# Kernel optimization log

Hardware: AMD Instinct MI355X
Metric: run time of the kernel (lower is better)

The kernel has to match this reference:

```python
import jax, jax.numpy as jnp
import numpy as np

N = 50000          # nodes
E = 1250000        # edges (no self loops in raw data)
H = 2              # heads
C = 32             # out channels per head
DIN = 64           # dim_node
ED = 16            # edge_dim
G = 16             # graphs in batch
NC = 5             # num classes
SLOPE = 0.2        # GATConv leaky_relu negative_slope


def _glorot(key, shape):
    fan = shape[0] if len(shape) == 2 else shape[-1]
    return jax.random.normal(key, shape, jnp.float32) * (1.0 / np.sqrt(fan))


def setup_inputs() -> dict:
    key = jax.random.key(0)
    ks = jax.random.split(key, 24)
    x = jax.random.normal(ks[0], (N, DIN), jnp.float32)
    dst = jax.random.randint(ks[1], (E,), 0, N)
    off = jax.random.randint(ks[2], (E,), 1, N)
    src = (dst + off) % N  # guarantees src != dst (PyG removes self loops before re-adding)
    edge_index = jnp.stack([src, dst]).astype(jnp.int32)
    edge_attr = jax.random.normal(ks[3], (E, ED), jnp.float32)
    batch = jnp.sort(jax.random.randint(ks[4], (N,), 0, G)).astype(jnp.int32)
    inp = dict(x=x, edge_index=edge_index, edge_attr=edge_attr, batch=batch)
    # layer 1: in=DIN, heads=H, out=C, concat -> H*C
    inp["W1"] = _glorot(ks[5], (DIN, H * C)); inp["asrc1"] = _glorot(ks[6], (H, C))
    inp["adst1"] = _glorot(ks[7], (H, C)); inp["We1"] = _glorot(ks[8], (ED, H * C))
    inp["ae1"] = _glorot(ks[9], (H, C)); inp["b1"] = jnp.zeros((H * C,), jnp.float32)
    # layer 2: in=H*C, heads=H, out=C, concat
    inp["W2"] = _glorot(ks[10], (H * C, H * C)); inp["asrc2"] = _glorot(ks[11], (H, C))
    inp["adst2"] = _glorot(ks[12], (H, C)); inp["We2"] = _glorot(ks[13], (ED, H * C))
    inp["ae2"] = _glorot(ks[14], (H, C)); inp["b2"] = jnp.zeros((H * C,), jnp.float32)
    # layer 3: in=H*C, heads=1, out=C, concat=False
    inp["W3"] = _glorot(ks[15], (H * C, C)); inp["asrc3"] = _glorot(ks[16], (1, C))
    inp["adst3"] = _glorot(ks[17], (1, C)); inp["We3"] = _glorot(ks[18], (ED, C))
    inp["ae3"] = _glorot(ks[19], (1, C)); inp["b3"] = jnp.zeros((C,), jnp.float32)
    # ffn: Linear(C, NC) + softmax (dropout is identity in eval)
    inp["Wf"] = _glorot(ks[20], (C, NC)); inp["bf"] = jnp.zeros((NC,), jnp.float32)
    return inp


def _gat_layer(h_in, src, dst, eattr, W, asrc, adst, We, ae, b, heads, out, concat):
    n = h_in.shape[0]
    h = (h_in @ W).reshape(n, heads, out)                      # [N,H,C]
    s_src = jnp.einsum('nhc,hc->nh', h, asrc)                  # per-node src scores
    s_dst = jnp.einsum('nhc,hc->nh', h, adst)
    he = (eattr @ We).reshape(-1, heads, out)                  # [E,H,C]
    s_e = jnp.einsum('ehc,hc->eh', he, ae)
    logit = jax.nn.leaky_relu(s_src[src] + s_dst[dst] + s_e, SLOPE)  # [E,H]
    m = jax.ops.segment_max(logit, dst, num_segments=n)
    ex = jnp.exp(logit - m[dst])
    den = jax.ops.segment_sum(ex, dst, num_segments=n)
    alpha = ex / (den[dst] + 1e-16)                            # segment softmax per dst node
    agg = jax.ops.segment_sum(h[src] * alpha[..., None], dst, num_segments=n)  # [N,H,C]
    out_x = agg.reshape(n, heads * out) if concat else agg.mean(axis=1)
    return out_x + b


def _gat_forward(x, edge_index, edge_attr, batch,
                 W1, asrc1, adst1, We1, ae1, b1,
                 W2, asrc2, adst2, We2, ae2, b2,
                 W3, asrc3, adst3, We3, ae3, b3,
                 Wf, bf):
    src, dst = edge_index[0], edge_index[1]
    n = x.shape[0]
    # add_self_loops with fill_value='mean': self-loop edge_attr = mean of incoming edge_attr
    deg = jax.ops.segment_sum(jnp.ones((src.shape[0],), x.dtype), dst, num_segments=n)
    self_attr = jax.ops.segment_sum(edge_attr, dst, num_segments=n) / jnp.maximum(deg, 1.0)[:, None]
    loop = jnp.arange(n, dtype=src.dtype)
    src_a = jnp.concatenate([src, loop])
    dst_a = jnp.concatenate([dst, loop])
    eattr_a = jnp.concatenate([edge_attr, self_attr], axis=0)

    h = jax.nn.relu(_gat_layer(x, src_a, dst_a, eattr_a, W1, asrc1, adst1, We1, ae1, b1, H, C, True))
    h = jax.nn.relu(_gat_layer(h, src_a, dst_a, eattr_a, W2, asrc2, adst2, We2, ae2, b2, H, C, True))
    h = jax.nn.relu(_gat_layer(h, src_a, dst_a, eattr_a, W3, asrc3, adst3, We3, ae3, b3, 1, C, False))

    # global mean pool per graph
    cnt = jax.ops.segment_sum(jnp.ones((n,), h.dtype), batch, num_segments=G)
    pooled = jax.ops.segment_sum(h, batch, num_segments=G) / jnp.maximum(cnt, 1.0)[:, None]
    # ffn: Dropout (identity at eval) -> Linear -> Softmax(dim=1)
    return jax.nn.softmax(pooled @ Wf + bf, axis=1)


def reference(x, edge_index, edge_attr, batch,
              W1, asrc1, adst1, We1, ae1, b1,
              W2, asrc2, adst2, We2, ae2, b2,
              W3, asrc3, adst3, We3, ae3, b3,
              Wf, bf):
    return _gat_forward(x, edge_index, edge_attr, batch,
                        W1, asrc1, adst1, We1, ae1, b1,
                        W2, asrc2, adst2, We2, ae2, b2,
                        W3, asrc3, adst3, We3, ae3, b3,
                        Wf, bf)
```

## Files before the change

### kernel.cpp

```cpp
#include <hip/hip_runtime.h>
#include <math.h>

#define NN 50000
#define EE 1250000
#define GG 16
#define NCLS 5
#define NBIN 391
#define BINSHIFT 7
#define CAPB 3900

constexpr size_t AL(size_t x){ return (x + 255) & ~size_t(255); }
constexpr size_t OFF_ROWPTR = 0;
constexpr size_t OFF_SRCS   = OFF_ROWPTR + AL((size_t)(NN+1)*4);
constexpr size_t OFF_SE12   = OFF_SRCS + AL((size_t)EE*2);
constexpr size_t OFF_SE34   = OFF_SE12 + AL((size_t)EE*4);
constexpr size_t OFF_SE5    = OFF_SE34 + AL((size_t)EE*4);
constexpr size_t OFF_SSRC   = OFF_SE5 + AL((size_t)EE*2);
constexpr size_t OFF_SDST   = OFF_SSRC + AL((size_t)NN*2*4);
constexpr size_t OFF_STAG   = OFF_SDST + AL((size_t)NN*2*4);
constexpr size_t OFF_BUFH   = OFF_STAG + AL((size_t)NBIN*CAPB*16);
constexpr size_t OFF_BUFO   = OFF_BUFH + AL((size_t)NN*32*4);
constexpr size_t OFF_POOL   = OFF_BUFO + AL((size_t)NN*64*4);

__device__ __forceinline__ float leaky(float x){ return x > 0.f ? x : 0.2f*x; }
__device__ __forceinline__ unsigned rne_bf16(float x){
    unsigned u = __float_as_uint(x);
    return (u + 0x7FFFu + ((u >> 16) & 1u)) >> 16;
}
__device__ __forceinline__ float bf16lo(unsigned p){ return __uint_as_float(p << 16); }
__device__ __forceinline__ float bf16hi(unsigned p){ return __uint_as_float(p & 0xFFFF0000u); }

__global__ void binA_kernel(const int* __restrict__ src, const int* __restrict__ dst,
                            const float* __restrict__ eattr,
                            const float* __restrict__ We1, const float* __restrict__ ae1,
                            const float* __restrict__ We2, const float* __restrict__ ae2,
                            const float* __restrict__ We3, const float* __restrict__ ae3,
                            int* __restrict__ bincursor, int4* __restrict__ staging, int nE){
    __shared__ int lcount[NBIN];
    __shared__ int lbase[NBIN];
    __shared__ float w[80];
    int tid = threadIdx.x;
    if (tid < 80){
        int j = tid >> 4, d = tid & 15;
        const float* We; const float* ae; int hc, h;
        if (j == 0){ We = We1; ae = ae1; hc = 64; h = 0; }
        else if (j == 1){ We = We1; ae = ae1; hc = 64; h = 1; }
        else if (j == 2){ We = We2; ae = ae2; hc = 64; h = 0; }
        else if (j == 3){ We = We2; ae = ae2; hc = 64; h = 1; }
        else { We = We3; ae = ae3; hc = 32; h = 0; }
        float s = 0.f;
        for (int c = 0; c < 32; ++c) s += We[d*hc + h*32 + c] * ae[h*32 + c];
        w[tid] = s;
    }
    for (int i = tid; i < NBIN; i += 1024) lcount[i] = 0;
    __syncthreads();
    int base = blockIdx.x * 2048;
    int w0[2], bn[2], idx[2]; unsigned p01[2], p23[2], p4[2];
    #pragma unroll
    for (int k = 0; k < 2; ++k){
        int i = base + k*1024 + tid;
        if (i < nE){
            int d = dst[i];
            int s = src[i];
            bn[k]  = d >> BINSHIFT;
            w0[k]  = s | ((d & 127) << 16);
            const float4* row = (const float4*)(eattr + (size_t)i*16);
            float4 a0 = row[0], a1 = row[1], a2 = row[2], a3 = row[3];
            float a[16] = {a0.x,a0.y,a0.z,a0.w, a1.x,a1.y,a1.z,a1.w,
                           a2.x,a2.y,a2.z,a2.w, a3.x,a3.y,a3.z,a3.w};
            float sj[5];
            #pragma unroll
            for (int j = 0; j < 5; ++j){
                float s2 = 0.f;
                #pragma unroll
                for (int d2 = 0; d2 < 16; ++d2) s2 += a[d2]*w[j*16+d2];
                sj[j] = s2;
            }
            p01[k] = rne_bf16(sj[0]) | (rne_bf16(sj[1]) << 16);
            p23[k] = rne_bf16(sj[2]) | (rne_bf16(sj[3]) << 16);
            p4[k]  = rne_bf16(sj[4]);
            idx[k] = atomicAdd(&lcount[bn[k]], 1);
        } else bn[k] = -1;
    }
    __syncthreads();
    for (int i = tid; i < NBIN; i += 1024){
        int c = lcount[i];
        lbase[i] = c ? (i*CAPB + atomicAdd(&bincursor[i], c)) : 0;
    }
    __syncthreads();
    #pragma unroll
    for (int k = 0; k < 2; ++k)
        if (bn[k] >= 0)
            staging[lbase[bn[k]] + idx[k]] = make_int4(w0[k], (int)p01[k], (int)p23[k], (int)p4[k]);
}

__global__ void binB_kernel(const int* __restrict__ bincursor, const int4* __restrict__ staging,
                            unsigned short* __restrict__ srcs, unsigned* __restrict__ se12,
                            unsigned* __restrict__ se34, unsigned short* __restrict__ se5,
                            int* __restrict__ rowptr, int nN){
    __shared__ int4 lout[CAPB];
    __shared__ int lcnt[128];
    __shared__ int lpre[128];
    __shared__ int sbb;
    int b = blockIdx.x;
    int sbase = b*CAPB;
    int cnt = bincursor[b];
    int tid = threadIdx.x;
    if (tid < 128) lcnt[tid] = 0;
    if (tid < 64){
        int sum = 0;
        for (int i = tid; i < b; i += 64) sum += bincursor[i];
        #pragma unroll
        for (int m = 1; m < 64; m <<= 1) sum += __shfl_xor(sum, m);
        if (tid == 0) sbb = sum;
    }
    __syncthreads();
    for (int k = tid; k < cnt; k += 1024)
        atomicAdd(&lcnt[staging[sbase + k].x >> 16], 1);
    __syncthreads();
    if (tid < 64){
        int a0 = lcnt[2*tid], a1 = lcnt[2*tid+1];
        int pair = a0 + a1, incl = pair;
        #pragma unroll
        for (int off = 1; off < 64; off <<= 1){
            int t = __shfl_up(incl, off);
            if (tid >= off) incl += t;
        }
        int base0 = incl - pair;
        lpre[2*tid] = base0;
        lpre[2*tid+1] = base0 + a0;
    }
    __syncthreads();
    int r0 = sbb;
    int lo = b << BINSHIFT;
    if (tid < 128 && lo + tid < nN) rowptr[lo + tid] = r0 + lpre[tid];
    if (b == 0 && tid == 0) rowptr[nN] = EE;
    if (tid < 128) lcnt[tid] = 0;
    __syncthreads();
    for (int k = tid; k < cnt; k += 1024){
        int4 v = staging[sbase + k];
        int dl = v.x >> 16;
        int rank = atomicAdd(&lcnt[dl], 1);
        v.x &= 0xFFFF;
        lout[lpre[dl] + rank] = v;
    }
    __syncthreads();
    for (int k = tid; k < cnt; k += 1024){
        int4 v = lout[k];
        srcs[r0 + k] = (unsigned short)v.x;
        se12[r0 + k] = (unsigned)v.y;
        se34[r0 + k] = (unsigned)v.z;
        se5[r0 + k]  = (unsigned short)v.w;
    }
}

template<int OUTC>
__global__ void transform_kernel(const float* __restrict__ in, const float* __restrict__ W,
                                 const float* __restrict__ asrc, const float* __restrict__ adst,
                                 unsigned* __restrict__ hout2, float* __restrict__ ssrc,
                                 float* __restrict__ sdst, int nN){
    constexpr int R = 256/OUTC;
    __shared__ float Ws[64*OUTC];
    __shared__ float ins[R*64];
    int tid = threadIdx.x;
    for (int i = tid; i < 64*OUTC; i += 256) Ws[i] = W[i];
    int base = blockIdx.x * R;
    for (int i = tid; i < R*64; i += 256){
        int n = base + i/64;
        ins[i] = (n < nN) ? in[(size_t)n*64 + (i & 63)] : 0.f;
    }
    __syncthreads();
    int r = tid / OUTC, c = tid % OUTC;
    int n = base + r;
    float acc = 0.f;
    #pragma unroll
    for (int d = 0; d < 64; ++d) acc += ins[r*64 + d] * Ws[d*OUTC + c];
    float ps = acc * asrc[c];
    float pd = acc * adst[c];
    #pragma unroll
    for (int m = 1; m <= 16; m <<= 1){ ps += __shfl_xor(ps, m); pd += __shfl_xor(pd, m); }
    float accN = __shfl_xor(acc, 1);
    if (n < nN){
        if ((c & 1) == 0){
            unsigned pk = rne_bf16(acc) | (rne_bf16(accN) << 16);
            hout2[(size_t)n*(OUTC/2) + (c >> 1)] = pk;
        }
        constexpr int HEADS = OUTC/32;
        if ((c & 31) == 0){
            int h = c >> 5;
            ssrc[n*HEADS + h] = ps;
            sdst[n*HEADS + h] = pd;
        }
    }
}

template<int OUTC>
__global__ void agg_kernel(const int* __restrict__ rowptr, const unsigned short* __restrict__ srcs,
                           const unsigned* __restrict__ sePa, const unsigned short* __restrict__ sePb,
                           const float* __restrict__ ssrc, const float* __restrict__ sdst,
                           const unsigned* __restrict__ hbuf2, const float* __restrict__ bias,
                           float* __restrict__ outbuf, int nN){
    constexpr int HEADS = OUTC/32;
    constexpr int HALF  = OUTC/4;
    constexpr int EPI   = 64/HALF;
    int wid = threadIdx.x >> 6;
    int lane = threadIdx.x & 63;
    int n = blockIdx.x*4 + wid;
    if (n >= nN) return;
    int row_start = rowptr[n], row_end = rowptr[n+1];
    int degn = row_end - row_start;
    float sd0 = sdst[n*HEADS + 0];
    float sd1 = (HEADS == 2) ? sdst[n*HEADS + 1] : 0.f;

    int sub = lane / HALF;
    int lc  = lane & (HALF - 1);
    int h   = (HEADS == 2) ? ((4*lc) >> 5) : 0;

    float acc0=0.f, acc1=0.f, acc2=0.f, acc3=0.f, den=0.f;
    float ssp0=0.f, ssp1=0.f;
    const uint2* hb2 = (const uint2*)hbuf2;

    for (int p0 = row_start; p0 < row_end; p0 += 64){
        int myp = p0 + lane;
        int srcreg = 0; unsigned wpk = 0; float w0s = 0.f;
        if (myp < row_end){
            srcreg = srcs[myp];
            if (HEADS == 2){
                unsigned pk = sePa[myp];
                float e0 = bf16lo(pk);
                float e1 = bf16hi(pk);
                ssp0 += e0; ssp1 += e1;
                float2 sv = ((const float2*)ssrc)[srcreg];
                float w0 = __expf(leaky(sv.x + sd0 + e0));
                float w1 = __expf(leaky(sv.y + sd1 + e1));
                wpk = rne_bf16(w0) | (rne_bf16(w1) << 16);
            } else {
                float e0 = __uint_as_float(((unsigned)sePb[myp]) << 16);
                ssp0 += e0;
                w0s = __expf(leaky(ssrc[srcreg] + sd0 + e0));
            }
        }
        int cnt = min(64, row_end - p0);
        #pragma unroll 2
        for (int q = sub; q < cnt; q += EPI){
            int sj = __shfl(srcreg, q);
            float wj;
            if (HEADS == 2){
                unsigned wq = __shfl(wpk, q);
                wj = h ? bf16hi(wq) : bf16lo(wq);
            } else {
                wj = __shfl(w0s, q);
            }
            den += wj;
            uint2 hv = hb2[(size_t)sj*(OUTC/4) + lc];
            acc0 += wj * bf16lo(hv.x);
            acc1 += wj * bf16hi(hv.x);
            acc2 += wj * bf16lo(hv.y);
            acc3 += wj * bf16hi(hv.y);
        }
    }

    #pragma unroll
    for (int m = HALF; m < 64; m <<= 1){
        acc0 += __shfl_xor(acc0, m); acc1 += __shfl_xor(acc1, m);
        acc2 += __shfl_xor(acc2, m); acc3 += __shfl_xor(acc3, m);
        den  += __shfl_xor(den, m);
    }
    #pragma unroll
    for (int m = 1; m < 64; m <<= 1){
        ssp0 += __shfl_xor(ssp0, m);
        if (HEADS == 2) ssp1 += __shfl_xor(ssp1, m);
    }

    float invdeg = 1.f / (float)max(degn, 1);
    float srh = ssrc[n*HEADS + h];
    float sdh = h ? sd1 : sd0;
    float ssh = h ? ssp1 : ssp0;
    float wself = __expf(leaky(srh + sdh + ssh*invdeg));
    uint2 hv = hb2[(size_t)n*(OUTC/4) + lc];
    acc0 += wself * bf16lo(hv.x); acc1 += wself * bf16hi(hv.x);
    acc2 += wself * bf16lo(hv.y); acc3 += wself * bf16hi(hv.y);
    den += wself;

    if (lane < HALF){
        float inv = 1.f / (den + 1e-16f);
        float4 o;
        o.x = fmaxf(acc0*inv + bias[4*lc+0], 0.f);
        o.y = fmaxf(acc1*inv + bias[4*lc+1], 0.f);
        o.z = fmaxf(acc2*inv + bias[4*lc+2], 0.f);
        o.w = fmaxf(acc3*inv + bias[4*lc+3], 0.f);
        ((float4*)outbuf)[(size_t)n*(OUTC/4) + lc] = o;
    }
}

__global__ void pool_kernel(const float* __restrict__ h3, const int* __restrict__ batch,
                            float* __restrict__ pool, float* __restrict__ cnt, int nN){
    __shared__ float accs[GG*32];
    __shared__ float acccnt[GG];
    int tid = threadIdx.x;
    for (int i = tid; i < GG*32; i += 256) accs[i] = 0.f;
    if (tid < GG) acccnt[tid] = 0.f;
    __syncthreads();
    int r = tid >> 5, c = tid & 31;
    int base = blockIdx.x * 512;
    int end = min(base + 512, nN);
    for (int n = base + r; n < end; n += 8){
        int g = batch[n];
        atomicAdd(&accs[g*32 + c], h3[(size_t)n*32 + c]);
        if (c == 0) atomicAdd(&acccnt[g], 1.f);
    }
    __syncthreads();
    for (int i = tid; i < GG*32; i += 256) atomicAdd(&pool[i], accs[i]);
    if (tid < GG) atomicAdd(&cnt[tid], acccnt[tid]);
}

__global__ void final_kernel(const float* __restrict__ pool, const float* __restrict__ cnt,
                             const float* __restrict__ Wf, const float* __restrict__ bf,
                             float* __restrict__ out){
    int g = threadIdx.x;
    if (g >= GG) return;
    float ic = 1.f / fmaxf(cnt[g], 1.f);
    float lg[NCLS];
    #pragma unroll
    for (int k = 0; k < NCLS; ++k) lg[k] = bf[k];
    for (int c = 0; c < 32; ++c){
        float v = pool[g*32 + c] * ic;
        #pragma unroll
        for (int k = 0; k < NCLS; ++k) lg[k] += v * Wf[c*NCLS + k];
    }
    float mx = lg[0];
    #pragma unroll
    for (int k = 1; k < NCLS; ++k) mx = fmaxf(mx, lg[k]);
    float sum = 0.f, ex[NCLS];
    #pragma unroll
    for (int k = 0; k < NCLS; ++k){ ex[k] = expf(lg[k] - mx); sum += ex[k]; }
    #pragma unroll
    for (int k = 0; k < NCLS; ++k) out[g*NCLS + k] = ex[k]/sum;
}

extern "C" void kernel_launch(void* const* d_in, const int* in_sizes, int n_in,
                              void* d_out, int out_size, void* d_ws, size_t ws_size,
                              hipStream_t stream){
    const float* x     = (const float*)d_in[0];
    const int*   eidx  = (const int*)d_in[1];
    const float* eattr = (const float*)d_in[2];
    const int*   batch = (const int*)d_in[3];
    const float* W1 = (const float*)d_in[4];  const float* asrc1 = (const float*)d_in[5];
    const float* adst1 = (const float*)d_in[6]; const float* We1 = (const float*)d_in[7];
    const float* ae1 = (const float*)d_in[8];  const float* b1 = (const float*)d_in[9];
    const float* W2 = (const float*)d_in[10]; const float* asrc2 = (const float*)d_in[11];
    const float* adst2 = (const float*)d_in[12]; const float* We2 = (const float*)d_in[13];
    const float* ae2 = (const float*)d_in[14]; const float* b2 = (const float*)d_in[15];
    const float* W3 = (const float*)d_in[16]; const float* asrc3 = (const float*)d_in[17];
    const float* adst3 = (const float*)d_in[18]; const float* We3 = (const float*)d_in[19];
    const float* ae3 = (const float*)d_in[20]; const float* b3 = (const float*)d_in[21];
    const float* Wf = (const float*)d_in[22]; const float* bf = (const float*)d_in[23];
    float* out = (float*)d_out;

    char* ws = (char*)d_ws;
    int*   rowptr = (int*)(ws + OFF_ROWPTR);
    unsigned short* srcs = (unsigned short*)(ws + OFF_SRCS);
    unsigned* se12 = (unsigned*)(ws + OFF_SE12);
    unsigned* se34 = (unsigned*)(ws + OFF_SE34);
    unsigned short* se5 = (unsigned short*)(ws + OFF_SE5);
    float* ssrc   = (float*)(ws + OFF_SSRC);
    float* sdst   = (float*)(ws + OFF_SDST);
    int4*  staging = (int4*)(ws + OFF_STAG);
    unsigned* bufH = (unsigned*)(ws + OFF_BUFH);
    float* bufO   = (float*)(ws + OFF_BUFO);
    float* pool   = (float*)(ws + OFF_POOL);
    float* cnt    = pool + GG*32;
    int*   bincursor = (int*)(cnt + GG);

    const int* srcA = eidx;
    const int* dstA = eidx + EE;

    hipMemsetAsync(pool, 0, (GG*32 + GG)*4 + NBIN*4, stream);

    binA_kernel<<<(EE + 2047)/2048, 1024, 0, stream>>>(srcA, dstA, eattr,
                                                       We1, ae1, We2, ae2, We3, ae3,
                                                       bincursor, staging, EE);
    binB_kernel<<<NBIN, 1024, 0, stream>>>(bincursor, staging, srcs, se12, se34, se5, rowptr, NN);

    int ngrid4 = (NN + 3)/4;
    int ngrid8 = (NN + 7)/8;
    transform_kernel<64><<<ngrid4, 256, 0, stream>>>(x, W1, asrc1, adst1, bufH, ssrc, sdst, NN);
    agg_kernel<64><<<ngrid4, 256, 0, stream>>>(rowptr, srcs, se12, nullptr,
                                               ssrc, sdst, bufH, b1, bufO, NN);
    transform_kernel<64><<<ngrid4, 256, 0, stream>>>(bufO, W2, asrc2, adst2, bufH, ssrc, sdst, NN);
    agg_kernel<64><<<ngrid4, 256, 0, stream>>>(rowptr, srcs, se34, nullptr,
                                               ssrc, sdst, bufH, b2, bufO, NN);
    transform_kernel<32><<<ngrid8, 256, 0, stream>>>(bufO, W3, asrc3, adst3, bufH, ssrc, sdst, NN);
    agg_kernel<32><<<ngrid4, 256, 0, stream>>>(rowptr, srcs, nullptr, se5,
                                               ssrc, sdst, bufH, b3, bufO, NN);
    pool_kernel<<<(NN + 511)/512, 256, 0, stream>>>(bufO, batch, pool, cnt, NN);
    final_kernel<<<1, 64, 0, stream>>>(pool, cnt, Wf, bf, out);
}
```

Measured before the change: 266.0 us.

## Fuse layer-1 transform into edge binning kernel as extra blocks

Merges the first-layer node transform into the edge binning pass. The launch gets extra blocks beyond the binning blocks, and each extra block computes x·W1, the attention logits and the bf16-packed features for 16 nodes. The point is to save one kernel launch and let the compute-bound transform overlap the memory-bound binning. It also raises the unroll factor in the aggregation inner loop. In exchange, the shared memory is now a union sized for the larger role, which can lower occupancy for the binning blocks, and the more aggressive unroll raises register pressure.

```diff
diff --git a/kernel.cpp b/kernel.cpp
--- a/kernel.cpp
+++ b/kernel.cpp
@@ -8,6 +8,8 @@
 #define NBIN 391
 #define BINSHIFT 7
 #define CAPB 3900
+#define NABLK 611
+#define NTBLK 3125
 
 constexpr size_t AL(size_t x){ return (x + 255) & ~size_t(255); }
 constexpr size_t OFF_ROWPTR = 0;
@@ -30,16 +32,57 @@
 __device__ __forceinline__ float bf16lo(unsigned p){ return __uint_as_float(p << 16); }
 __device__ __forceinline__ float bf16hi(unsigned p){ return __uint_as_float(p & 0xFFFF0000u); }
 
-__global__ void binA_kernel(const int* __restrict__ src, const int* __restrict__ dst,
-                            const float* __restrict__ eattr,
-                            const float* __restrict__ We1, const float* __restrict__ ae1,
-                            const float* __restrict__ We2, const float* __restrict__ ae2,
-                            const float* __restrict__ We3, const float* __restrict__ ae3,
-                            int* __restrict__ bincursor, int4* __restrict__ staging, int nE){
-    __shared__ int lcount[NBIN];
-    __shared__ int lbase[NBIN];
-    __shared__ float w[80];
+__global__ __launch_bounds__(1024)
+void binAt1_kernel(const int* __restrict__ src, const int* __restrict__ dst,
+                   const float* __restrict__ eattr,
+                   const float* __restrict__ We1, const float* __restrict__ ae1,
+                   const float* __restrict__ We2, const float* __restrict__ ae2,
+                   const float* __restrict__ We3, const float* __restrict__ ae3,
+                   int* __restrict__ bincursor, int4* __restrict__ staging,
+                   const float* __restrict__ x, const float* __restrict__ W1,
+                   const float* __restrict__ asrc1, const float* __restrict__ adst1,
+                   unsigned* __restrict__ hout2, float* __restrict__ ssrc,
+                   float* __restrict__ sdst, int nE, int nN){
+    __shared__ float smem[5120];
     int tid = threadIdx.x;
+
+    if (blockIdx.x >= NABLK){
+        float* Ws  = smem;
+        float* ins = smem + 4096;
+        for (int i = tid; i < 4096; i += 1024) Ws[i] = W1[i];
+        int base = (blockIdx.x - NABLK) * 16;
+        {
+            int n = base + (tid >> 6);
+            ins[tid] = (n < nN) ? x[(size_t)n*64 + (tid & 63)] : 0.f;
+        }
+        __syncthreads();
+        int r = tid >> 6, c = tid & 63;
+        int n = base + r;
+        float acc = 0.f;
+        #pragma unroll
+        for (int d = 0; d < 64; ++d) acc += ins[r*64 + d] * Ws[d*64 + c];
+        float ps = acc * asrc1[c];
+        float pd = acc * adst1[c];
+        #pragma unroll
+        for (int m = 1; m <= 16; m <<= 1){ ps += __shfl_xor(ps, m); pd += __shfl_xor(pd, m); }
+        float accN = __shfl_xor(acc, 1);
+        if (n < nN){
+            if ((c & 1) == 0){
+                unsigned pk = rne_bf16(acc) | (rne_bf16(accN) << 16);
+                hout2[(size_t)n*32 + (c >> 1)] = pk;
+            }
+            if ((c & 31) == 0){
+                int h = c >> 5;
+                ssrc[n*2 + h] = ps;
+                sdst[n*2 + h] = pd;
+            }
+        }
+        return;
+    }
+
+    int*   lcount = (int*)smem;
+    int*   lbase  = lcount + NBIN;
+    float* w      = (float*)(lbase + NBIN);
     if (tid < 80){
         int j = tid >> 4, d = tid & 15;
         const float* We; const float* ae; int hc, h;
@@ -241,7 +284,7 @@
             }
         }
         int cnt = min(64, row_end - p0);
-        #pragma unroll 2
+        #pragma unroll 4
         for (int q = sub; q < cnt; q += EPI){
             int sj = __shfl(srcreg, q);
             float wj;
@@ -377,14 +420,15 @@
 
     hipMemsetAsync(pool, 0, (GG*32 + GG)*4 + NBIN*4, stream);
 
-    binA_kernel<<<(EE + 2047)/2048, 1024, 0, stream>>>(srcA, dstA, eattr,
-                                                       We1, ae1, We2, ae2, We3, ae3,
-                                                       bincursor, staging, EE);
+    binAt1_kernel<<<NABLK + NTBLK, 1024, 0, stream>>>(srcA, dstA, eattr,
+                                                      We1, ae1, We2, ae2, We3, ae3,
+                                                      bincursor, staging,
+                                                      x, W1, asrc1, adst1,
+                                                      bufH, ssrc, sdst, EE, NN);
     binB_kernel<<<NBIN, 1024, 0, stream>>>(bincursor, staging, srcs, se12, se34, se5, rowptr, NN);
 
     int ngrid4 = (NN + 3)/4;
     int ngrid8 = (NN + 7)/8;
-    transform_kernel<64><<<ngrid4, 256, 0, stream>>>(x, W1, asrc1, adst1, bufH, ssrc, sdst, NN);
     agg_kernel<64><<<ngrid4, 256, 0, stream>>>(rowptr, srcs, se12, nullptr,
                                                ssrc, sdst, bufH, b1, bufO, NN);
     transform_kernel<64><<<ngrid4, 256, 0, stream>>>(bufO, W2, asrc2, adst2, bufH, ssrc, sdst, NN);
```

New measurement: 261.9 us. About the same (-1.5%).
